# Kernel optimization log

Hardware: AMD Instinct MI355X
Metric: run time of the kernel (lower is better)

Reference implementation:

```python
import jax, jax.numpy as jnp
import numpy as np

N = 100000      # n_nodes
D = 64          # d_model
E = 1_600_000   # n_edges
L = 3           # n_layers


def setup_inputs() -> dict:
    key = jax.random.key(0)
    ks = jax.random.split(key, 2 + 2 * L)
    x = jax.random.normal(ks[0], (N, D), dtype=jnp.float32)
    edge_index = jax.random.randint(ks[1], (2, E), 0, N, dtype=jnp.int32)
    inp = {"x": x, "edge_index": edge_index}
    scale = 1.0 / np.sqrt(D)
    for i in range(L):
        # GCNConv weight (glorot-ish init) and zero bias
        inp[f"W{i}"] = jax.random.uniform(ks[2 + 2 * i], (D, D), jnp.float32, -scale, scale)
        inp[f"b{i}"] = jnp.zeros((D,), jnp.float32)
    return inp


def gcn_conv(x, W, b, src, dst, num_nodes):
    # PyG GCNConv: h = x @ W, then D^{-1/2}(A+I)D^{-1/2} aggregation, then + b
    h = x @ W  # [N, D]
    ones = jnp.ones(dst.shape, dtype=h.dtype)
    deg = jax.ops.segment_sum(ones, dst, num_segments=num_nodes)  # [N]
    deg_inv_sqrt = jnp.where(deg > 0, jax.lax.rsqrt(jnp.maximum(deg, 1.0)), 0.0)
    norm = deg_inv_sqrt[src] * deg_inv_sqrt[dst]  # [E+N]
    msg = h[src] * norm[:, None]                  # gather + scale  [E+N, D]
    out = jax.ops.segment_sum(msg, dst, num_segments=num_nodes)  # scatter-add [N, D]
    return out + b


def reference(x, edge_index, W0, b0, W1, b1, W2, b2):
    num_nodes = x.shape[0]
    loop = jnp.arange(num_nodes, dtype=edge_index.dtype)
    src = jnp.concatenate([edge_index[0], loop])  # add self-loops
    dst = jnp.concatenate([edge_index[1], loop])
    h = x
    for W, b in ((W0, b0), (W1, b1), (W2, b2)):
        h = gcn_conv(h, W, b, src, dst, num_nodes)
        # F.dropout(training=self.training) is identity in eval mode
    return h
```

## Files before the change

kernel.cpp:

```cpp
#include <hip/hip_runtime.h>
#include <hip/hip_bf16.h>

#define D 64
#define RSHIFT 9
#define BNODES 512
#define MAXB 256
#define BCAP 10240
#define FH 72

typedef unsigned short ushort_t;
typedef unsigned int uint_t;
typedef short short8 __attribute__((ext_vector_type(8)));
typedef float floatx4 __attribute__((ext_vector_type(4)));

__device__ inline uint_t pk_bf16(float x, float y) {
    uint_t ux = __float_as_uint(x); ux = ux + 0x7fffu + ((ux >> 16) & 1u);
    uint_t uy = __float_as_uint(y); uy = uy + 0x7fffu + ((uy >> 16) & 1u);
    return (ux >> 16) | (uy & 0xffff0000u);
}
__device__ inline ushort_t rnd_bf16(float x) {
    uint_t u = __float_as_uint(x); u = u + 0x7fffu + ((u >> 16) & 1u);
    return (ushort_t)(u >> 16);
}

__global__ __launch_bounds__(256) void k_bucket(const int* __restrict__ src,
                                                const int* __restrict__ dst,
                                                int* __restrict__ bcur,
                                                int* __restrict__ ebuf,
                                                int E, int nb) {
    __shared__ int lcnt[MAXB];
    __shared__ int lbase[MAXB];
    int t = threadIdx.x;
    lcnt[t] = 0;
    __syncthreads();
    int base = blockIdx.x * 2048 + t * 8;
    int sv[8], dv[8], sl[8];
    if (base + 7 < E) {
        int4 a0 = *(const int4*)(src + base);
        int4 a1 = *(const int4*)(src + base + 4);
        int4 b0 = *(const int4*)(dst + base);
        int4 b1 = *(const int4*)(dst + base + 4);
        sv[0]=a0.x; sv[1]=a0.y; sv[2]=a0.z; sv[3]=a0.w;
        sv[4]=a1.x; sv[5]=a1.y; sv[6]=a1.z; sv[7]=a1.w;
        dv[0]=b0.x; dv[1]=b0.y; dv[2]=b0.z; dv[3]=b0.w;
        dv[4]=b1.x; dv[5]=b1.y; dv[6]=b1.z; dv[7]=b1.w;
    } else {
        #pragma unroll
        for (int j = 0; j < 8; ++j) {
            dv[j] = (base + j < E) ? dst[base + j] : -1;
            sv[j] = (base + j < E) ? src[base + j] : 0;
        }
    }
    #pragma unroll
    for (int j = 0; j < 8; ++j) {
        if (dv[j] >= 0) {
            int b = dv[j] >> RSHIFT;
            sl[j] = atomicAdd(&lcnt[b], 1);
        }
    }
    __syncthreads();
    if (t < nb) { int c = lcnt[t]; if (c) lbase[t] = atomicAdd(&bcur[t], c); }
    __syncthreads();
    #pragma unroll
    for (int j = 0; j < 8; ++j) {
        if (dv[j] >= 0) {
            int b = dv[j] >> RSHIFT;
            int slot = lbase[b] + sl[j];
            if (slot < BCAP)
                ebuf[(size_t)b * BCAP + slot] = (sv[j] << RSHIFT) | (dv[j] & (BNODES - 1));
        }
    }
}

__global__ __launch_bounds__(256) void k_csr(const int* __restrict__ ebuf,
                                             const int* __restrict__ bcur,
                                             int* __restrict__ rowptr,
                                             int* __restrict__ ssrc,
                                             float* __restrict__ dis,
                                             int N, int nb) {
    __shared__ int lcnt[BNODES];
    __shared__ int lcur[BNODES];
    __shared__ int sums[256];
    __shared__ int red[4];
    int b = blockIdx.x;
    int t = threadIdx.x;
    int n = bcur[b];
    int node0 = b << RSHIFT;
    int pv = (t < b) ? bcur[t] : 0;
    int lane = t & 63, w = t >> 6;
    #pragma unroll
    for (int off = 1; off < 64; off <<= 1) pv += __shfl_xor(pv, off, 64);
    if (lane == 0) red[w] = pv;
    #pragma unroll
    for (int i = t; i < BNODES; i += 256) lcnt[i] = 0;
    __syncthreads();
    int base = red[0] + red[1] + red[2] + red[3];
    const int* seg = ebuf + (size_t)b * BCAP;
    for (int i = t * 4; i < n; i += 1024) {
        if (i + 3 < n) {
            int4 e = *(const int4*)(seg + i);
            atomicAdd(&lcnt[e.x & (BNODES - 1)], 1);
            atomicAdd(&lcnt[e.y & (BNODES - 1)], 1);
            atomicAdd(&lcnt[e.z & (BNODES - 1)], 1);
            atomicAdd(&lcnt[e.w & (BNODES - 1)], 1);
        } else {
            for (int j = 0; j < 4 && i + j < n; ++j)
                atomicAdd(&lcnt[seg[i + j] & (BNODES - 1)], 1);
        }
    }
    __syncthreads();
    int idx = t * 2;
    int v0 = lcnt[idx], v1 = lcnt[idx + 1];
    int s = v0 + v1;
    sums[t] = s;
    __syncthreads();
    for (int off = 1; off < 256; off <<= 1) {
        int x = (t >= off) ? sums[t - off] : 0;
        __syncthreads();
        sums[t] += x;
        __syncthreads();
    }
    int run = sums[t] - s;
    int node = node0 + idx;
    lcur[idx] = base + run;
    if (node < N) { rowptr[node] = base + run; dis[node] = rsqrtf((float)(v0 + 1)); }
    run += v0;
    lcur[idx + 1] = base + run;
    if (node + 1 < N) { rowptr[node + 1] = base + run; dis[node + 1] = rsqrtf((float)(v1 + 1)); }
    if (b == nb - 1 && t == 0) rowptr[N] = base + n;
    __syncthreads();
    for (int i = t * 4; i < n; i += 1024) {
        if (i + 3 < n) {
            int4 e = *(const int4*)(seg + i);
            int p0 = atomicAdd(&lcur[e.x & (BNODES - 1)], 1); ssrc[p0] = e.x >> RSHIFT;
            int p1 = atomicAdd(&lcur[e.y & (BNODES - 1)], 1); ssrc[p1] = e.y >> RSHIFT;
            int p2 = atomicAdd(&lcur[e.z & (BNODES - 1)], 1); ssrc[p2] = e.z >> RSHIFT;
            int p3 = atomicAdd(&lcur[e.w & (BNODES - 1)], 1); ssrc[p3] = e.w >> RSHIFT;
        } else {
            for (int j = 0; j < 4 && i + j < n; ++j) {
                int e = seg[i + j];
                int p = atomicAdd(&lcur[e & (BNODES - 1)], 1); ssrc[p] = e >> RSHIFT;
            }
        }
    }
}

__device__ __forceinline__ void stage_wt(const float* __restrict__ W,
                                         ushort_t* __restrict__ wt, int t) {
    const float4* W4 = (const float4*)W;
    for (int i = t; i < 1024; i += 256) {
        float4 w4 = W4[i];
        int k = i >> 4, n0 = (i & 15) * 4;
        wt[(n0 + 0) * FH + k] = rnd_bf16(w4.x);
        wt[(n0 + 1) * FH + k] = rnd_bf16(w4.y);
        wt[(n0 + 2) * FH + k] = rnd_bf16(w4.z);
        wt[(n0 + 3) * FH + k] = rnd_bf16(w4.w);
    }
}

__global__ __launch_bounds__(256) void k_gemm0(const float* __restrict__ x,
                                               const float* __restrict__ W,
                                               const float* __restrict__ dis,
                                               ushort_t* __restrict__ G, int N) {
    __shared__ ushort_t wt[64 * FH];
    int t = threadIdx.x;
    stage_wt(W, wt, t);
    __syncthreads();
    int wv = t >> 6, lane = t & 63;
    int m = lane & 15, quad = lane >> 4;
    int row = blockIdx.x * 64 + wv * 16 + m;
    long rowc = (row < N) ? row : (N - 1);
    float4 f0 = *(const float4*)(x + rowc * D + quad * 8);
    float4 f1 = *(const float4*)(x + rowc * D + quad * 8 + 4);
    float4 f2 = *(const float4*)(x + rowc * D + 32 + quad * 8);
    float4 f3 = *(const float4*)(x + rowc * D + 32 + quad * 8 + 4);
    union { short8 s; uint_t u[4]; } a0, a1;
    a0.u[0] = pk_bf16(f0.x, f0.y); a0.u[1] = pk_bf16(f0.z, f0.w);
    a0.u[2] = pk_bf16(f1.x, f1.y); a0.u[3] = pk_bf16(f1.z, f1.w);
    a1.u[0] = pk_bf16(f2.x, f2.y); a1.u[1] = pk_bf16(f2.z, f2.w);
    a1.u[2] = pk_bf16(f3.x, f3.y); a1.u[3] = pk_bf16(f3.z, f3.w);
    floatx4 acc[4];
    #pragma unroll
    for (int j = 0; j < 4; ++j) {
        short8 b0 = *(short8*)&wt[(j * 16 + m) * FH + quad * 8];
        short8 b1 = *(short8*)&wt[(j * 16 + m) * FH + 32 + quad * 8];
        floatx4 z = {0.f, 0.f, 0.f, 0.f};
        acc[j] = __builtin_amdgcn_mfma_f32_16x16x32_bf16(a0.s, b0, z, 0, 0, 0);
        acc[j] = __builtin_amdgcn_mfma_f32_16x16x32_bf16(a1.s, b1, acc[j], 0, 0, 0);
    }
    int rbase = blockIdx.x * 64 + wv * 16 + quad * 4;
    #pragma unroll
    for (int r = 0; r < 4; ++r) {
        int rr = rbase + r;
        if (rr < N) {
            float sc = dis[rr];
            #pragma unroll
            for (int j = 0; j < 4; ++j)
                G[(size_t)rr * D + j * 16 + m] = rnd_bf16(acc[j][r] * sc);
        }
    }
}

__device__ __forceinline__ void gather_node(const ushort_t* __restrict__ G,
                                            const int* __restrict__ ssrc,
                                            int beg, int end, int c8,
                                            int node, float a[8]) {
    uint4 su = *(const uint4*)(G + (size_t)node * D + c8);
    a[0] = __uint_as_float(su.x << 16);
    a[1] = __uint_as_float(su.x & 0xffff0000u);
    a[2] = __uint_as_float(su.y << 16);
    a[3] = __uint_as_float(su.y & 0xffff0000u);
    a[4] = __uint_as_float(su.z << 16);
    a[5] = __uint_as_float(su.z & 0xffff0000u);
    a[6] = __uint_as_float(su.w << 16);
    a[7] = __uint_as_float(su.w & 0xffff0000u);
    #define ACCUM(u)                                                       \
        {                                                                  \
            a[0] += __uint_as_float(u.x << 16);                            \
            a[1] += __uint_as_float(u.x & 0xffff0000u);                    \
            a[2] += __uint_as_float(u.y << 16);                            \
            a[3] += __uint_as_float(u.y & 0xffff0000u);                    \
            a[4] += __uint_as_float(u.z << 16);                            \
            a[5] += __uint_as_float(u.z & 0xffff0000u);                    \
            a[6] += __uint_as_float(u.w << 16);                            \
            a[7] += __uint_as_float(u.w & 0xffff0000u);                    \
        }
    int e = beg;
    int n8 = (end - beg) >> 3;
    if (n8 > 0) {
        int s0 = ssrc[e], s1 = ssrc[e + 1], s2 = ssrc[e + 2], s3 = ssrc[e + 3];
        int s4 = ssrc[e + 4], s5 = ssrc[e + 5], s6 = ssrc[e + 6], s7 = ssrc[e + 7];
        for (int ch = 0; ch < n8; ++ch) {
            int ne = e + 8;
            int t0 = s0, t1 = s1, t2 = s2, t3 = s3, t4 = s4, t5 = s5, t6 = s6, t7 = s7;
            if (ch + 1 < n8) {
                s0 = ssrc[ne];     s1 = ssrc[ne + 1]; s2 = ssrc[ne + 2]; s3 = ssrc[ne + 3];
                s4 = ssrc[ne + 4]; s5 = ssrc[ne + 5]; s6 = ssrc[ne + 6]; s7 = ssrc[ne + 7];
            }
            uint4 u0 = *(const uint4*)(G + (size_t)t0 * D + c8);
            uint4 u1 = *(const uint4*)(G + (size_t)t1 * D + c8);
            uint4 u2 = *(const uint4*)(G + (size_t)t2 * D + c8);
            uint4 u3 = *(const uint4*)(G + (size_t)t3 * D + c8);
            uint4 u4 = *(const uint4*)(G + (size_t)t4 * D + c8);
            uint4 u5 = *(const uint4*)(G + (size_t)t5 * D + c8);
            uint4 u6 = *(const uint4*)(G + (size_t)t6 * D + c8);
            uint4 u7 = *(const uint4*)(G + (size_t)t7 * D + c8);
            ACCUM(u0); ACCUM(u1); ACCUM(u2); ACCUM(u3);
            ACCUM(u4); ACCUM(u5); ACCUM(u6); ACCUM(u7);
            e = ne;
        }
    }
    if (e + 4 <= end) {
        int s0 = ssrc[e], s1 = ssrc[e + 1], s2 = ssrc[e + 2], s3 = ssrc[e + 3];
        uint4 u0 = *(const uint4*)(G + (size_t)s0 * D + c8);
        uint4 u1 = *(const uint4*)(G + (size_t)s1 * D + c8);
        uint4 u2 = *(const uint4*)(G + (size_t)s2 * D + c8);
        uint4 u3 = *(const uint4*)(G + (size_t)s3 * D + c8);
        ACCUM(u0); ACCUM(u1); ACCUM(u2); ACCUM(u3);
        e += 4;
    }
    if (e + 2 <= end) {
        int s0 = ssrc[e], s1 = ssrc[e + 1];
        uint4 u0 = *(const uint4*)(G + (size_t)s0 * D + c8);
        uint4 u1 = *(const uint4*)(G + (size_t)s1 * D + c8);
        ACCUM(u0); ACCUM(u1);
        e += 2;
    }
    if (e < end) {
        int s0 = ssrc[e];
        uint4 u0 = *(const uint4*)(G + (size_t)s0 * D + c8);
        ACCUM(u0);
    }
    #undef ACCUM
}

__global__ __launch_bounds__(256) void k_fagg(const ushort_t* __restrict__ G,
                                              const float* __restrict__ dis,
                                              const int* __restrict__ rowptr,
                                              const int* __restrict__ ssrc,
                                              const float* __restrict__ bias,
                                              const float* __restrict__ W,
                                              ushort_t* __restrict__ Gout,
                                              int N) {
    __shared__ ushort_t hbuf[64 * FH];
    __shared__ ushort_t wt[64 * FH];
    int t = threadIdx.x;
    stage_wt(W, wt, t);
    int wv = t >> 6, lane = t & 63;
    int g = lane >> 3;
    int c8 = (lane & 7) * 8;
    int gbase = blockIdx.x * 64;
    float4 bv0 = *(const float4*)(bias + c8);
    float4 bv1 = *(const float4*)(bias + c8 + 4);
    for (int ii = 0; ii < 2; ++ii) {
        int idx = wv * 16 + ii * 8 + g;
        int node = gbase + idx;
        if (node < N) {
            int beg = rowptr[node], end = rowptr[node + 1];
            float di = dis[node];
            float a[8];
            gather_node(G, ssrc, beg, end, c8, node, a);
            uint4 p;
            p.x = pk_bf16(a[0] * di + bv0.x, a[1] * di + bv0.y);
            p.y = pk_bf16(a[2] * di + bv0.z, a[3] * di + bv0.w);
            p.z = pk_bf16(a[4] * di + bv1.x, a[5] * di + bv1.y);
            p.w = pk_bf16(a[6] * di + bv1.z, a[7] * di + bv1.w);
            *(uint4*)&hbuf[idx * FH + c8] = p;
        }
    }
    __syncthreads();
    int m = lane & 15, quad = lane >> 4;
    short8 a0 = *(short8*)&hbuf[(wv * 16 + m) * FH + quad * 8];
    short8 a1 = *(short8*)&hbuf[(wv * 16 + m) * FH + 32 + quad * 8];
    floatx4 acc[4];
    #pragma unroll
    for (int j = 0; j < 4; ++j) {
        short8 b0 = *(short8*)&wt[(j * 16 + m) * FH + quad * 8];
        short8 b1 = *(short8*)&wt[(j * 16 + m) * FH + 32 + quad * 8];
        floatx4 z = {0.f, 0.f, 0.f, 0.f};
        acc[j] = __builtin_amdgcn_mfma_f32_16x16x32_bf16(a0, b0, z, 0, 0, 0);
        acc[j] = __builtin_amdgcn_mfma_f32_16x16x32_bf16(a1, b1, acc[j], 0, 0, 0);
    }
    int rbase = gbase + wv * 16 + quad * 4;
    #pragma unroll
    for (int r = 0; r < 4; ++r) {
        int row = rbase + r;
        if (row < N) {
            float sc = dis[row];
            #pragma unroll
            for (int j = 0; j < 4; ++j)
                Gout[(size_t)row * D + j * 16 + m] = rnd_bf16(acc[j][r] * sc);
        }
    }
}

__global__ __launch_bounds__(256) void k_agg(const ushort_t* __restrict__ G,
                                             const float* __restrict__ dis,
                                             const int* __restrict__ rowptr,
                                             const int* __restrict__ ssrc,
                                             const float* __restrict__ bias,
                                             float* __restrict__ out, int N) {
    int t = threadIdx.x;
    int wv = t >> 6, lane = t & 63;
    int g = lane >> 3;
    int c8 = (lane & 7) * 8;
    int node = blockIdx.x * 32 + wv * 8 + g;
    if (node >= N) return;
    int beg = rowptr[node], end = rowptr[node + 1];
    float di = dis[node];
    float a[8];
    gather_node(G, ssrc, beg, end, c8, node, a);
    float4 bv0 = *(const float4*)(bias + c8);
    float4 bv1 = *(const float4*)(bias + c8 + 4);
    float4 r0, r1;
    r0.x = a[0] * di + bv0.x; r0.y = a[1] * di + bv0.y;
    r0.z = a[2] * di + bv0.z; r0.w = a[3] * di + bv0.w;
    r1.x = a[4] * di + bv1.x; r1.y = a[5] * di + bv1.y;
    r1.z = a[6] * di + bv1.z; r1.w = a[7] * di + bv1.w;
    float4* op = (float4*)(out + (size_t)node * D + c8);
    op[0] = r0;
    op[1] = r1;
}


extern "C" void kernel_launch(void* const* d_in, const int* in_sizes, int n_in,
                              void* d_out, int out_size, void* d_ws, size_t ws_size,
                              hipStream_t stream) {
    const float* x  = (const float*)d_in[0];
    const int*   ei = (const int*)d_in[1];
    const float* W0 = (const float*)d_in[2];
    const float* b0 = (const float*)d_in[3];
    const float* W1 = (const float*)d_in[4];
    const float* b1 = (const float*)d_in[5];
    const float* W2 = (const float*)d_in[6];
    const float* b2 = (const float*)d_in[7];
    float* out = (float*)d_out;

    const int N = in_sizes[0] / D;
    const int E = in_sizes[1] / 2;
    const int* e_src = ei;
    const int* e_dst = ei + E;

    ushort_t* B0   = (ushort_t*)d_ws;
    ushort_t* B1   = B0 + (size_t)N * D;
    float* dis     = (float*)(B1 + (size_t)N * D);
    int*   rowptr  = (int*)(dis + N);
    int*   ssrc    = rowptr + (N + 1);
    int*   bcur    = ssrc + E;
    int*   ebuf    = (int*)d_ws;

    const int nb = (N + BNODES - 1) >> RSHIFT;
    const int gG64 = (N + 63) / 64;
    const int gAgg = (N + 31) / 32;

    hipMemsetAsync(bcur, 0, MAXB * sizeof(int), stream);
    k_bucket<<<(E + 2047) / 2048, 256, 0, stream>>>(e_src, e_dst, bcur, ebuf, E, nb);
    k_csr<<<nb, 256, 0, stream>>>(ebuf, bcur, rowptr, ssrc, dis, N, nb);

    k_gemm0<<<gG64, 256, 0, stream>>>(x, W0, dis, B0, N);
    k_fagg<<<gG64, 256, 0, stream>>>(B0, dis, rowptr, ssrc, b0, W1, B1, N);
    k_fagg<<<gG64, 256, 0, stream>>>(B1, dis, rowptr, ssrc, b1, W2, B0, N);
    k_agg<<<gAgg, 256, 0, stream>>>(B0, dis, rowptr, ssrc, b2, out, N);
}
```

Measured before the change: 254.6 us.

## Pad CSR rows to multiples of eight with dummy zero row and octant-ordered sources

Each node's neighbor list is padded to a multiple of 8 entries that point to an extra all-zero row N, which removes the tail handling in the gather loop and allows int4 index loads. Row extents become per-bucket fixed-capacity segments stored as int2 begin/end, so the global prefix over buckets is no longer needed. Within each row, sources are emitted in eight passes over a shared-memory copy of the bucket, grouped by source-id octant, to improve locality of the gathers. The cost is extra padded gather work, eight passes in the CSR build, a larger ssrc buffer, and silent truncation if a bucket exceeds its capacity.

```diff
diff --git a/kernel.cpp b/kernel.cpp
--- a/kernel.cpp
+++ b/kernel.cpp
@@ -6,6 +6,9 @@
 #define BNODES 512
 #define MAXB 256
 #define BCAP 10240
+#define SCAP 14336
+#define OCT_SHIFT 14
+#define NOCT 8
 #define FH 72
 
 typedef unsigned short ushort_t;
@@ -74,44 +77,45 @@
 
 __global__ __launch_bounds__(256) void k_csr(const int* __restrict__ ebuf,
                                              const int* __restrict__ bcur,
-                                             int* __restrict__ rowptr,
+                                             int2* __restrict__ rowse,
                                              int* __restrict__ ssrc,
                                              float* __restrict__ dis,
                                              int N, int nb) {
+    __shared__ int sseg[BCAP];
     __shared__ int lcnt[BNODES];
     __shared__ int lcur[BNODES];
     __shared__ int sums[256];
-    __shared__ int red[4];
     int b = blockIdx.x;
     int t = threadIdx.x;
     int n = bcur[b];
+    if (n > BCAP) n = BCAP;
     int node0 = b << RSHIFT;
-    int pv = (t < b) ? bcur[t] : 0;
-    int lane = t & 63, w = t >> 6;
-    #pragma unroll
-    for (int off = 1; off < 64; off <<= 1) pv += __shfl_xor(pv, off, 64);
-    if (lane == 0) red[w] = pv;
     #pragma unroll
     for (int i = t; i < BNODES; i += 256) lcnt[i] = 0;
     __syncthreads();
-    int base = red[0] + red[1] + red[2] + red[3];
     const int* seg = ebuf + (size_t)b * BCAP;
     for (int i = t * 4; i < n; i += 1024) {
         if (i + 3 < n) {
             int4 e = *(const int4*)(seg + i);
+            *(int4*)(sseg + i) = e;
             atomicAdd(&lcnt[e.x & (BNODES - 1)], 1);
             atomicAdd(&lcnt[e.y & (BNODES - 1)], 1);
             atomicAdd(&lcnt[e.z & (BNODES - 1)], 1);
             atomicAdd(&lcnt[e.w & (BNODES - 1)], 1);
         } else {
-            for (int j = 0; j < 4 && i + j < n; ++j)
-                atomicAdd(&lcnt[seg[i + j] & (BNODES - 1)], 1);
+            for (int j = 0; j < 4 && i + j < n; ++j) {
+                int e = seg[i + j];
+                sseg[i + j] = e;
+                atomicAdd(&lcnt[e & (BNODES - 1)], 1);
+            }
         }
     }
     __syncthreads();
     int idx = t * 2;
     int v0 = lcnt[idx], v1 = lcnt[idx + 1];
-    int s = v0 + v1;
+    int p0 = (v0 + 7) & ~7;
+    int p1 = (v1 + 7) & ~7;
+    int s = p0 + p1;
     sums[t] = s;
     __syncthreads();
     for (int off = 1; off < 256; off <<= 1) {
@@ -121,28 +125,27 @@
         __syncthreads();
     }
     int run = sums[t] - s;
+    int beg0 = b * SCAP + run;
+    int beg1 = beg0 + p0;
+    lcur[idx] = beg0;
+    lcur[idx + 1] = beg1;
     int node = node0 + idx;
-    lcur[idx] = base + run;
-    if (node < N) { rowptr[node] = base + run; dis[node] = rsqrtf((float)(v0 + 1)); }
-    run += v0;
-    lcur[idx + 1] = base + run;
-    if (node + 1 < N) { rowptr[node + 1] = base + run; dis[node + 1] = rsqrtf((float)(v1 + 1)); }
-    if (b == nb - 1 && t == 0) rowptr[N] = base + n;
-    __syncthreads();
-    for (int i = t * 4; i < n; i += 1024) {
-        if (i + 3 < n) {
-            int4 e = *(const int4*)(seg + i);
-            int p0 = atomicAdd(&lcur[e.x & (BNODES - 1)], 1); ssrc[p0] = e.x >> RSHIFT;
-            int p1 = atomicAdd(&lcur[e.y & (BNODES - 1)], 1); ssrc[p1] = e.y >> RSHIFT;
-            int p2 = atomicAdd(&lcur[e.z & (BNODES - 1)], 1); ssrc[p2] = e.z >> RSHIFT;
-            int p3 = atomicAdd(&lcur[e.w & (BNODES - 1)], 1); ssrc[p3] = e.w >> RSHIFT;
-        } else {
-            for (int j = 0; j < 4 && i + j < n; ++j) {
-                int e = seg[i + j];
-                int p = atomicAdd(&lcur[e & (BNODES - 1)], 1); ssrc[p] = e >> RSHIFT;
+    if (node < N)     { rowse[node]     = make_int2(beg0, beg0 + p0); dis[node]     = rsqrtf((float)(v0 + 1)); }
+    if (node + 1 < N) { rowse[node + 1] = make_int2(beg1, beg1 + p1); dis[node + 1] = rsqrtf((float)(v1 + 1)); }
+    __syncthreads();
+    for (int oc = 0; oc < NOCT; ++oc) {
+        for (int i = t; i < n; i += 256) {
+            int e = sseg[i];
+            int sv = e >> RSHIFT;
+            if ((sv >> OCT_SHIFT) == oc) {
+                int p = atomicAdd(&lcur[e & (BNODES - 1)], 1);
+                ssrc[p] = sv;
             }
         }
-    }
+        __syncthreads();
+    }
+    for (int k = v0; k < p0; ++k) ssrc[beg0 + k] = N;
+    for (int k = v1; k < p1; ++k) ssrc[beg1 + k] = N;
 }
 
 __device__ __forceinline__ void stage_wt(const float* __restrict__ W,
@@ -225,18 +228,14 @@
             a[6] += __uint_as_float(u.w << 16);                            \
             a[7] += __uint_as_float(u.w & 0xffff0000u);                    \
         }
-    int e = beg;
     int n8 = (end - beg) >> 3;
+    const int4* sp = (const int4*)(ssrc + beg);
     if (n8 > 0) {
-        int s0 = ssrc[e], s1 = ssrc[e + 1], s2 = ssrc[e + 2], s3 = ssrc[e + 3];
-        int s4 = ssrc[e + 4], s5 = ssrc[e + 5], s6 = ssrc[e + 6], s7 = ssrc[e + 7];
+        int4 ia = sp[0], ib = sp[1];
         for (int ch = 0; ch < n8; ++ch) {
-            int ne = e + 8;
-            int t0 = s0, t1 = s1, t2 = s2, t3 = s3, t4 = s4, t5 = s5, t6 = s6, t7 = s7;
-            if (ch + 1 < n8) {
-                s0 = ssrc[ne];     s1 = ssrc[ne + 1]; s2 = ssrc[ne + 2]; s3 = ssrc[ne + 3];
-                s4 = ssrc[ne + 4]; s5 = ssrc[ne + 5]; s6 = ssrc[ne + 6]; s7 = ssrc[ne + 7];
-            }
+            int t0 = ia.x, t1 = ia.y, t2 = ia.z, t3 = ia.w;
+            int t4 = ib.x, t5 = ib.y, t6 = ib.z, t7 = ib.w;
+            if (ch + 1 < n8) { ia = sp[2 * ch + 2]; ib = sp[2 * ch + 3]; }
             uint4 u0 = *(const uint4*)(G + (size_t)t0 * D + c8);
             uint4 u1 = *(const uint4*)(G + (size_t)t1 * D + c8);
             uint4 u2 = *(const uint4*)(G + (size_t)t2 * D + c8);
@@ -247,36 +246,14 @@
             uint4 u7 = *(const uint4*)(G + (size_t)t7 * D + c8);
             ACCUM(u0); ACCUM(u1); ACCUM(u2); ACCUM(u3);
             ACCUM(u4); ACCUM(u5); ACCUM(u6); ACCUM(u7);
-            e = ne;
-        }
-    }
-    if (e + 4 <= end) {
-        int s0 = ssrc[e], s1 = ssrc[e + 1], s2 = ssrc[e + 2], s3 = ssrc[e + 3];
-        uint4 u0 = *(const uint4*)(G + (size_t)s0 * D + c8);
-        uint4 u1 = *(const uint4*)(G + (size_t)s1 * D + c8);
-        uint4 u2 = *(const uint4*)(G + (size_t)s2 * D + c8);
-        uint4 u3 = *(const uint4*)(G + (size_t)s3 * D + c8);
-        ACCUM(u0); ACCUM(u1); ACCUM(u2); ACCUM(u3);
-        e += 4;
-    }
-    if (e + 2 <= end) {
-        int s0 = ssrc[e], s1 = ssrc[e + 1];
-        uint4 u0 = *(const uint4*)(G + (size_t)s0 * D + c8);
-        uint4 u1 = *(const uint4*)(G + (size_t)s1 * D + c8);
-        ACCUM(u0); ACCUM(u1);
-        e += 2;
-    }
-    if (e < end) {
-        int s0 = ssrc[e];
-        uint4 u0 = *(const uint4*)(G + (size_t)s0 * D + c8);
-        ACCUM(u0);
+        }
     }
     #undef ACCUM
 }
 
 __global__ __launch_bounds__(256) void k_fagg(const ushort_t* __restrict__ G,
                                               const float* __restrict__ dis,
-                                              const int* __restrict__ rowptr,
+                                              const int2* __restrict__ rowse,
                                               const int* __restrict__ ssrc,
                                               const float* __restrict__ bias,
                                               const float* __restrict__ W,
@@ -296,10 +273,10 @@
         int idx = wv * 16 + ii * 8 + g;
         int node = gbase + idx;
         if (node < N) {
-            int beg = rowptr[node], end = rowptr[node + 1];
+            int2 se = rowse[node];
             float di = dis[node];
             float a[8];
-            gather_node(G, ssrc, beg, end, c8, node, a);
+            gather_node(G, ssrc, se.x, se.y, c8, node, a);
             uint4 p;
             p.x = pk_bf16(a[0] * di + bv0.x, a[1] * di + bv0.y);
             p.y = pk_bf16(a[2] * di + bv0.z, a[3] * di + bv0.w);
@@ -336,7 +313,7 @@
 
 __global__ __launch_bounds__(256) void k_agg(const ushort_t* __restrict__ G,
                                              const float* __restrict__ dis,
-                                             const int* __restrict__ rowptr,
+                                             const int2* __restrict__ rowse,
                                              const int* __restrict__ ssrc,
                                              const float* __restrict__ bias,
                                              float* __restrict__ out, int N) {
@@ -346,10 +323,10 @@
     int c8 = (lane & 7) * 8;
     int node = blockIdx.x * 32 + wv * 8 + g;
     if (node >= N) return;
-    int beg = rowptr[node], end = rowptr[node + 1];
+    int2 se = rowse[node];
     float di = dis[node];
     float a[8];
-    gather_node(G, ssrc, beg, end, c8, node, a);
+    gather_node(G, ssrc, se.x, se.y, c8, node, a);
     float4 bv0 = *(const float4*)(bias + c8);
     float4 bv1 = *(const float4*)(bias + c8 + 4);
     float4 r0, r1;
@@ -381,24 +358,29 @@
     const int* e_src = ei;
     const int* e_dst = ei + E;
 
+    const int nb = (N + BNODES - 1) >> RSHIFT;
+
+    size_t rowsz   = (size_t)(N + 1) * D;
     ushort_t* B0   = (ushort_t*)d_ws;
-    ushort_t* B1   = B0 + (size_t)N * D;
-    float* dis     = (float*)(B1 + (size_t)N * D);
-    int*   rowptr  = (int*)(dis + N);
-    int*   ssrc    = rowptr + (N + 1);
-    int*   bcur    = ssrc + E;
+    ushort_t* B1   = B0 + rowsz;
+    float* dis     = (float*)(B1 + rowsz);
+    int2*  rowse   = (int2*)(dis + N);
+    int*   ssrc    = (int*)(rowse + N);
+    int*   bcur    = ssrc + (size_t)nb * SCAP;
     int*   ebuf    = (int*)d_ws;
 
-    const int nb = (N + BNODES - 1) >> RSHIFT;
     const int gG64 = (N + 63) / 64;
     const int gAgg = (N + 31) / 32;
 
     hipMemsetAsync(bcur, 0, MAXB * sizeof(int), stream);
+    hipMemsetAsync(B0 + (size_t)N * D, 0, D * sizeof(ushort_t), stream);
+    hipMemsetAsync(B1 + (size_t)N * D, 0, D * sizeof(ushort_t), stream);
+
     k_bucket<<<(E + 2047) / 2048, 256, 0, stream>>>(e_src, e_dst, bcur, ebuf, E, nb);
-    k_csr<<<nb, 256, 0, stream>>>(ebuf, bcur, rowptr, ssrc, dis, N, nb);
+    k_csr<<<nb, 256, 0, stream>>>(ebuf, bcur, rowse, ssrc, dis, N, nb);
 
     k_gemm0<<<gG64, 256, 0, stream>>>(x, W0, dis, B0, N);
-    k_fagg<<<gG64, 256, 0, stream>>>(B0, dis, rowptr, ssrc, b0, W1, B1, N);
-    k_fagg<<<gG64, 256, 0, stream>>>(B1, dis, rowptr, ssrc, b1, W2, B0, N);
-    k_agg<<<gAgg, 256, 0, stream>>>(B0, dis, rowptr, ssrc, b2, out, N);
-}
+    k_fagg<<<gG64, 256, 0, stream>>>(B0, dis, rowse, ssrc, b0, W1, B1, N);
+    k_fagg<<<gG64, 256, 0, stream>>>(B1, dis, rowse, ssrc, b1, W2, B0, N);
+    k_agg<<<gAgg, 256, 0, stream>>>(B0, dis, rowse, ssrc, b2, out, N);
+}
```

Result: no change. 258.4 us (+1.5%).
